# Performance work log

Measured on AMD Instinct MI355X. Metric: run time of the kernel, lower is better.

## Reference

```python
import jax, jax.numpy as jnp
import numpy as np
import math

B, N, DIM = 2, 4096, 1024
H, D, M = 16, 64, 256


def setup_inputs() -> dict:
    key = jax.random.key(0)
    ks = jax.random.split(key, 6)
    s = 1.0 / math.sqrt(DIM)
    return {
        "x": jax.random.normal(ks[0], (B, N, DIM), dtype=jnp.float32),
        "w_q": jax.random.normal(ks[1], (DIM, H * D), dtype=jnp.float32) * s,
        "w_k": jax.random.normal(ks[2], (DIM, H * D), dtype=jnp.float32) * s,
        "w_v": jax.random.normal(ks[3], (DIM, H * D), dtype=jnp.float32) * s,
        "w_o": jax.random.normal(ks[4], (H * D, DIM), dtype=jnp.float32) * s,
        "b_o": jnp.zeros((DIM,), dtype=jnp.float32),
        "omega": jax.random.normal(ks[5], (M, D), dtype=jnp.float32),
    }


def _heads(t):
    # [B, N, H*D] -> [B, H, N, D]
    return t.reshape(B, N, H, D).transpose(0, 2, 1, 3)


def _phi(t, omega):
    # t: [B,H,N,D], omega: [M,D] -> [B,H,N,M]
    proj = jnp.einsum("bhnd,md->bhnm", t, omega)
    norm = 0.5 * jnp.sum(t * t, axis=-1, keepdims=True)
    return jnp.exp(proj - norm) / math.sqrt(M)


def reference(x, w_q, w_k, w_v, w_o, b_o, omega):
    q = _heads(x @ w_q)
    k = _heads(x @ w_k)
    v = _heads(x @ w_v)
    phi_q = _phi(q, omega)          # [B,H,N,M]
    phi_k = _phi(k, omega)          # [B,H,N,M]
    kv = jnp.einsum("bhnm,bhnd->bhmd", phi_k, v)   # [B,H,M,D]
    k_sum = phi_k.sum(axis=2)                       # [B,H,M]
    z = 1.0 / (jnp.einsum("bhnm,bhm->bhn", phi_q, k_sum) + 1e-6)
    out = jnp.einsum("bhnm,bhmd->bhnd", phi_q, kv) * z[..., None]
    out = out.transpose(0, 2, 1, 3).reshape(B, N, H * D)
    return out @ w_o + b_o
```

## Files before the change

### kernel.cpp

```cpp
#include <hip/hip_runtime.h>

#define DEVI __device__ __forceinline__

using f32x4 = __attribute__((ext_vector_type(4))) float;
using fvec4 = __attribute__((ext_vector_type(4))) float;
using s16x4 = __attribute__((ext_vector_type(4))) short;
using s16x8 = __attribute__((ext_vector_type(8))) short;

DEVI unsigned short f2bf_rn(float f) {
  union { float f; unsigned u; } v; v.f = f;
  unsigned r = v.u + 0x7fffu + ((v.u >> 16) & 1u);
  return (unsigned short)(r >> 16);
}
DEVI float bf2f(unsigned short h) {
  union { unsigned u; float f; } v; v.u = ((unsigned)h) << 16;
  return v.f;
}
DEVI f32x4 mfma16(s16x8 a, s16x8 b, f32x4 c) {
  return __builtin_amdgcn_mfma_f32_16x16x32_bf16(a, b, c, 0, 0, 0);
}
DEVI void gld16(const void* g, void* lds) {
  __builtin_amdgcn_global_load_lds(
      (const __attribute__((address_space(1))) unsigned int*)g,
      (__attribute__((address_space(3))) unsigned int*)lds, 16, 0, 0);
}

__global__ __launch_bounds__(256) void k_split_x(
    const float* __restrict__ X,
    unsigned short* __restrict__ XH, unsigned short* __restrict__ XL)
{
  size_t i = ((size_t)blockIdx.x * 256 + threadIdx.x) * 8;
  fvec4 a = *(const fvec4*)&X[i];
  fvec4 b = *(const fvec4*)&X[i + 4];
  s16x8 hv, lv;
#pragma unroll
  for (int j = 0; j < 4; ++j) {
    unsigned short h = f2bf_rn(a[j]);
    hv[j] = (short)h; lv[j] = (short)f2bf_rn(a[j] - bf2f(h));
  }
#pragma unroll
  for (int j = 0; j < 4; ++j) {
    unsigned short h = f2bf_rn(b[j]);
    hv[4 + j] = (short)h; lv[4 + j] = (short)f2bf_rn(b[j] - bf2f(h));
  }
  *(s16x8*)&XH[i] = hv;
  *(s16x8*)&XL[i] = lv;
}

__global__ __launch_bounds__(256) void k_prep_w(
    const float* __restrict__ wq, const float* __restrict__ wk,
    const float* __restrict__ wv, const float* __restrict__ wo,
    unsigned short* __restrict__ WTh, unsigned short* __restrict__ WOT)
{
  __shared__ float tile[64][65];
  const int z = blockIdx.z;
  const float* src = (z == 0) ? wq : (z == 1) ? wk : (z == 2) ? wv : wo;
  const int k0 = blockIdx.x * 64;
  const int n0 = blockIdx.y * 64;
  const int t = threadIdx.x;
#pragma unroll
  for (int j = 0; j < 4; ++j) {
    int r = (t >> 4) + 16 * j;
    int c = (t & 15) * 4;
    fvec4 v = *(const fvec4*)&src[(size_t)(k0 + r) * 1024 + n0 + c];
#pragma unroll
    for (int i = 0; i < 4; ++i) tile[r][c + i] = v[i];
  }
  __syncthreads();
#pragma unroll
  for (int j = 0; j < 4; ++j) {
    int n = (t >> 4) + 16 * j;
    int kc = (t & 15) * 4;
    s16x4 hv;
#pragma unroll
    for (int i = 0; i < 4; ++i) hv[i] = (short)f2bf_rn(tile[kc + i][n]);
    if (z < 3) {
      *(s16x4*)&WTh[(size_t)(z * 1024 + n0 + n) * 1024 + k0 + kc] = hv;
    } else {
      *(s16x4*)&WOT[(size_t)(n0 + n) * 1024 + k0 + kc] = hv;
    }
  }
}

__global__ __launch_bounds__(256) void k_gemm_qkv(
    const unsigned short* __restrict__ XH, const unsigned short* __restrict__ XL,
    const unsigned short* __restrict__ WTh,
    unsigned short* __restrict__ QH, unsigned short* __restrict__ QL,
    unsigned short* __restrict__ KH, unsigned short* __restrict__ KL,
    unsigned short* __restrict__ VB)
{
  __shared__ unsigned short AH[2][128 * 32];
  __shared__ unsigned short BHs[2][128 * 32];
  __shared__ unsigned short AL[2][128 * 32];
  const int flat = blockIdx.y * 24 + blockIdx.x;
  const int swz = (flat & 7) * 192 + (flat >> 3);
  const int cb = swz % 24;
  const int rb = swz / 24;
  const int t = threadIdx.x;
  const int w = t >> 6, l = t & 63;
  const bool tp = (cb < 16);
  f32x4 acc[4][4];
#pragma unroll
  for (int a = 0; a < 4; ++a)
#pragma unroll
    for (int b = 0; b < 4; ++b) acc[a][b] = (f32x4)0.f;

  const int r0 = w * 32;
  const int lrow = l >> 2;
  const int lcol = (l & 3) * 8;
  const size_t gA = (size_t)(rb * 128 + r0 + lrow) * 1024 + lcol;
  const size_t gB = (size_t)(cb * 128 + r0 + lrow) * 1024 + lcol;
  const int lds0 = r0 * 32;
  const int lds1 = (r0 + 16) * 32;

  const int wm = (w & 1) * 64, wn = (w >> 1) * 64;
  const int lr = l & 15, ko = (l >> 4) * 8;

  auto STAGE = [&](int buf, int k0) {
    gld16(&XH[gA + k0], &AH[buf][lds0]);
    gld16(&XH[gA + (size_t)16 * 1024 + k0], &AH[buf][lds1]);
    if (tp) {
      gld16(&XL[gA + k0], &AL[buf][lds0]);
      gld16(&XL[gA + (size_t)16 * 1024 + k0], &AL[buf][lds1]);
    }
    gld16(&WTh[gB + k0], &BHs[buf][lds0]);
    gld16(&WTh[gB + (size_t)16 * 1024 + k0], &BHs[buf][lds1]);
  };

  STAGE(0, 0);
  int cur = 0;
  for (int ks = 0; ks < 32; ++ks) {
    if (ks < 31) {
      STAGE(cur ^ 1, (ks + 1) * 32);
      if (tp) asm volatile("s_waitcnt vmcnt(6)" ::: "memory");
      else    asm volatile("s_waitcnt vmcnt(4)" ::: "memory");
    } else {
      asm volatile("s_waitcnt vmcnt(0)" ::: "memory");
    }
    __builtin_amdgcn_s_barrier();
    asm volatile("" ::: "memory");
    s16x8 ah[4], al[4], bh[4];
#pragma unroll
    for (int f = 0; f < 4; ++f) {
      ah[f] = *(const s16x8*)&AH[cur][(wm + f * 16 + lr) * 32 + ko];
      bh[f] = *(const s16x8*)&BHs[cur][(wn + f * 16 + lr) * 32 + ko];
    }
    if (tp) {
#pragma unroll
      for (int f = 0; f < 4; ++f) al[f] = *(const s16x8*)&AL[cur][(wm + f * 16 + lr) * 32 + ko];
    }
#pragma unroll
    for (int fa = 0; fa < 4; ++fa)
#pragma unroll
      for (int fb = 0; fb < 4; ++fb) {
        acc[fa][fb] = mfma16(ah[fa], bh[fb], acc[fa][fb]);
        if (tp) acc[fa][fb] = mfma16(al[fa], bh[fb], acc[fa][fb]);
      }
    asm volatile("s_waitcnt lgkmcnt(0)" ::: "memory");
    __builtin_amdgcn_s_barrier();
    asm volatile("" ::: "memory");
    cur ^= 1;
  }
  const int lg = l >> 4;
#pragma unroll
  for (int fa = 0; fa < 4; ++fa)
#pragma unroll
    for (int r = 0; r < 4; ++r) {
      int row = rb * 128 + wm + fa * 16 + lg * 4 + r;
#pragma unroll
      for (int fb = 0; fb < 4; ++fb) {
        int col = cb * 128 + wn + fb * 16 + lr;
        float v = acc[fa][fb][r];
        if (tp) {
          unsigned short hs = f2bf_rn(v);
          unsigned short ls = f2bf_rn(v - bf2f(hs));
          if (cb < 8) {
            QH[(size_t)row * 1024 + col] = hs;
            QL[(size_t)row * 1024 + col] = ls;
          } else {
            KH[(size_t)row * 1024 + col - 1024] = hs;
            KL[(size_t)row * 1024 + col - 1024] = ls;
          }
        } else {
          VB[(size_t)row * 1024 + col - 2048] = f2bf_rn(v);
        }
      }
    }
}

__global__ __launch_bounds__(512, 1) void k_phik_kv(
    const unsigned short* __restrict__ KH, const unsigned short* __restrict__ KL,
    const unsigned short* __restrict__ VB,
    const float* __restrict__ omega, float* __restrict__ KVP)
{
  __shared__ unsigned short OH[256][72];
  __shared__ unsigned short KHs[64][72], KLs[64][72];
  __shared__ unsigned short PKT[256][72];
  __shared__ unsigned short AVT[80][72];
  __shared__ float norm_s[64];
  const int nc = blockIdx.x;
  const int bh = blockIdx.y;
  const int b = bh >> 4, h = bh & 15;
  const int t = threadIdx.x, w = t >> 6, l = t & 63;
  const int lr = l & 15, lg = l >> 4, ko8 = lg * 8;

#pragma unroll
  for (int j = 0; j < 8; ++j) {
    int e = j * 512 + t;
    int m = e >> 4, c = (e & 15) * 4;
    fvec4 v = *(const fvec4*)&omega[m * 64 + c];
    s16x4 hv;
#pragma unroll
    for (int i = 0; i < 4; ++i) hv[i] = (short)f2bf_rn(v[i]);
    *(s16x4*)&OH[m][c] = hv;
  }
  for (int e = t; e < 16 * 64; e += 512) {
    int rr = e >> 6, cc = e & 63;
    AVT[64 + rr][cc] = (rr == 0) ? (unsigned short)0x3F80 : (unsigned short)0;
  }

  f32x4 acc2[5][2];
#pragma unroll
  for (int a = 0; a < 5; ++a)
#pragma unroll
    for (int bb = 0; bb < 2; ++bb) acc2[a][bb] = (f32x4)0.f;

  for (int st = 0; st < 8; ++st) {
    const int n0 = nc * 512 + st * 64;
    __syncthreads();
    {
      int r = t >> 3, c8 = (t & 7) * 8;
      size_t o = (size_t)(b * 4096 + n0 + r) * 1024 + h * 64 + c8;
      s16x8 vh = *(const s16x8*)&KH[o];
      s16x8 vl = *(const s16x8*)&KL[o];
      *(s16x8*)&KHs[r][c8] = vh;
      *(s16x8*)&KLs[r][c8] = vl;
      float ss = 0.f;
#pragma unroll
      for (int i = 0; i < 8; ++i) {
        float q = bf2f((unsigned short)vh[i]) + bf2f((unsigned short)vl[i]);
        ss += q * q;
      }
      ss += __shfl_xor(ss, 1);
      ss += __shfl_xor(ss, 2);
      ss += __shfl_xor(ss, 4);
      if ((t & 7) == 0) norm_s[r] = 0.5f * ss;
    }
    {
      int n = t >> 3, dq = (t & 7) * 8;
      s16x8 v = *(const s16x8*)&VB[(size_t)(b * 4096 + n0 + n) * 1024 + h * 64 + dq];
#pragma unroll
      for (int i = 0; i < 8; ++i) AVT[dq + i][n] = (unsigned short)v[i];
    }
    __syncthreads();
    f32x4 acc[4][2];
#pragma unroll
    for (int a = 0; a < 4; ++a)
#pragma unroll
      for (int bb = 0; bb < 2; ++bb) acc[a][bb] = (f32x4)0.f;
#pragma unroll
    for (int ksub = 0; ksub < 2; ++ksub) {
      int ko = ksub * 32 + ko8;
      s16x8 ah[4], al[4], bh[2];
#pragma unroll
      for (int f = 0; f < 4; ++f) {
        ah[f] = *(const s16x8*)&KHs[f * 16 + lr][ko];
        al[f] = *(const s16x8*)&KLs[f * 16 + lr][ko];
      }
#pragma unroll
      for (int f = 0; f < 2; ++f) bh[f] = *(const s16x8*)&OH[w * 32 + f * 16 + lr][ko];
#pragma unroll
      for (int fa = 0; fa < 4; ++fa)
#pragma unroll
        for (int fb = 0; fb < 2; ++fb) {
          acc[fa][fb] = mfma16(ah[fa], bh[fb], acc[fa][fb]);
          acc[fa][fb] = mfma16(al[fa], bh[fb], acc[fa][fb]);
        }
    }
#pragma unroll
    for (int fa = 0; fa < 4; ++fa)
#pragma unroll
      for (int r = 0; r < 4; ++r) {
        int n = fa * 16 + lg * 4 + r;
        float nm = norm_s[n];
#pragma unroll
        for (int fb = 0; fb < 2; ++fb) {
          int m = w * 32 + fb * 16 + lr;
          float p = __expf(acc[fa][fb][r] - nm) * 0.0625f;
          PKT[m][n] = f2bf_rn(p);
        }
      }
    __syncthreads();
#pragma unroll
    for (int ksub = 0; ksub < 2; ++ksub) {
      int ko = ksub * 32 + ko8;
      s16x8 fA[5], fB[2];
#pragma unroll
      for (int f = 0; f < 5; ++f) fA[f] = *(const s16x8*)&AVT[f * 16 + lr][ko];
#pragma unroll
      for (int f = 0; f < 2; ++f) fB[f] = *(const s16x8*)&PKT[w * 32 + f * 16 + lr][ko];
#pragma unroll
      for (int fa = 0; fa < 5; ++fa)
#pragma unroll
        for (int fb = 0; fb < 2; ++fb) acc2[fa][fb] = mfma16(fA[fa], fB[fb], acc2[fa][fb]);
    }
  }
#pragma unroll
  for (int fa = 0; fa < 5; ++fa)
#pragma unroll
    for (int r = 0; r < 4; ++r) {
      int dp = fa * 16 + lg * 4 + r;
#pragma unroll
      for (int fb = 0; fb < 2; ++fb) {
        int m = w * 32 + fb * 16 + lr;
        KVP[(size_t)((bh * 8 + nc) * 80 + dp) * 256 + m] = acc2[fa][fb][r];
      }
    }
}

__global__ __launch_bounds__(256) void k_kv_reduce(
    const float* __restrict__ KVP, float* __restrict__ KVT)
{
  int idx = blockIdx.x * 256 + threadIdx.x;
  if (idx >= 32 * 80 * 256) return;
  int bh = idx / (80 * 256);
  int rem = idx % (80 * 256);
  float s = 0.f;
#pragma unroll
  for (int nci = 0; nci < 8; ++nci) s += KVP[(size_t)(bh * 8 + nci) * 80 * 256 + rem];
  KVT[idx] = s;
}

__global__ __launch_bounds__(256) void k_phiq_attn(
    const unsigned short* QH, const unsigned short* QL,
    const float* __restrict__ omega, const float* __restrict__ KVT,
    unsigned short* ATT)
{
  __shared__ unsigned short QHs[64][72], QLs[64][72];
  __shared__ unsigned short OH[256][72];
  __shared__ unsigned short PQ[64][264];
  __shared__ unsigned short KVB[80][264];
  __shared__ float norm_s[64];
  const int nt = blockIdx.x;
  const int bh = blockIdx.y;
  const int t = threadIdx.x, w = t >> 6, l = t & 63;
  const int b = bh >> 4, h = bh & 15;
  const int lr = l & 15, lg = l >> 4, ko8 = lg * 8;

  {
    int r = t >> 2, cq = (t & 3) * 4;
    float ss = 0.f;
#pragma unroll
    for (int j = 0; j < 4; ++j) {
      int c = cq + 16 * j;
      size_t o = (size_t)(b * 4096 + nt * 64 + r) * 1024 + h * 64 + c;
      s16x4 vh = *(const s16x4*)&QH[o];
      s16x4 vl = *(const s16x4*)&QL[o];
      *(s16x4*)&QHs[r][c] = vh;
      *(s16x4*)&QLs[r][c] = vl;
#pragma unroll
      for (int i = 0; i < 4; ++i) {
        float q = bf2f((unsigned short)vh[i]) + bf2f((unsigned short)vl[i]);
        ss += q * q;
      }
    }
    ss += __shfl_xor(ss, 1);
    ss += __shfl_xor(ss, 2);
    if ((t & 3) == 0) norm_s[r] = 0.5f * ss;
  }
#pragma unroll
  for (int j = 0; j < 16; ++j) {
    int e = j * 256 + t;
    int m = e >> 4, c = (e & 15) * 4;
    fvec4 v = *(const fvec4*)&omega[m * 64 + c];
    s16x4 hv;
#pragma unroll
    for (int i = 0; i < 4; ++i) hv[i] = (short)f2bf_rn(v[i]);
    *(s16x4*)&OH[m][c] = hv;
  }
#pragma unroll
  for (int j = 0; j < 20; ++j) {
    int e = (j * 256 + t) * 4;
    int dp = e >> 8, m = e & 255;
    fvec4 v = *(const fvec4*)&KVT[(size_t)bh * 80 * 256 + dp * 256 + m];
    s16x4 hv;
#pragma unroll
    for (int i = 0; i < 4; ++i) hv[i] = (short)f2bf_rn(v[i]);
    *(s16x4*)&KVB[dp][m] = hv;
  }
  __syncthreads();
  f32x4 acc[4][4];
#pragma unroll
  for (int a = 0; a < 4; ++a)
#pragma unroll
    for (int bb = 0; bb < 4; ++bb) acc[a][bb] = (f32x4)0.f;
#pragma unroll
  for (int ksub = 0; ksub < 2; ++ksub) {
    int ko = ksub * 32 + ko8;
    s16x8 ah[4], al[4], bh[4];
#pragma unroll
    for (int f = 0; f < 4; ++f) {
      ah[f] = *(const s16x8*)&QHs[f * 16 + lr][ko];
      al[f] = *(const s16x8*)&QLs[f * 16 + lr][ko];
      bh[f] = *(const s16x8*)&OH[w * 64 + f * 16 + lr][ko];
    }
#pragma unroll
    for (int fa = 0; fa < 4; ++fa)
#pragma unroll
      for (int fb = 0; fb < 4; ++fb) {
        acc[fa][fb] = mfma16(ah[fa], bh[fb], acc[fa][fb]);
        acc[fa][fb] = mfma16(al[fa], bh[fb], acc[fa][fb]);
      }
  }
#pragma unroll
  for (int fa = 0; fa < 4; ++fa)
#pragma unroll
    for (int r = 0; r < 4; ++r) {
      int n = fa * 16 + lg * 4 + r;
      float nm = norm_s[n];
#pragma unroll
      for (int fb = 0; fb < 4; ++fb) {
        int m = w * 64 + fb * 16 + lr;
        float p = __expf(acc[fa][fb][r] - nm) * 0.0625f;
        PQ[n][m] = f2bf_rn(p);
      }
    }
  __syncthreads();
  f32x4 acc2[5];
#pragma unroll
  for (int bb = 0; bb < 5; ++bb) acc2[bb] = (f32x4)0.f;
  for (int ks = 0; ks < 8; ++ks) {
    const int m0 = ks * 32;
    s16x8 fA = *(const s16x8*)&PQ[w * 16 + lr][m0 + ko8];
    s16x8 fB[5];
#pragma unroll
    for (int f = 0; f < 5; ++f) fB[f] = *(const s16x8*)&KVB[f * 16 + lr][m0 + ko8];
#pragma unroll
    for (int fb = 0; fb < 5; ++fb) acc2[fb] = mfma16(fA, fB[fb], acc2[fb]);
  }
#pragma unroll
  for (int r = 0; r < 4; ++r) {
    float den = __shfl(acc2[4][r], (l & 48));
    float z = 1.f / (den + 1e-6f);
    int n = nt * 64 + w * 16 + lg * 4 + r;
#pragma unroll
    for (int fb = 0; fb < 4; ++fb) {
      int col = h * 64 + fb * 16 + lr;
      ATT[(size_t)(b * 4096 + n) * 1024 + col] = f2bf_rn(acc2[fb][r] * z);
    }
  }
}

__global__ __launch_bounds__(256) void k_gemm_out(
    const unsigned short* __restrict__ ATT,
    const unsigned short* __restrict__ WOT,
    const float* __restrict__ b_o,
    float* __restrict__ OUT)
{
  __shared__ unsigned short As[2][128 * 32], Bs[2][128 * 32];
  const int flat = blockIdx.y * 8 + blockIdx.x;
  const int swz = (flat & 7) * 64 + (flat >> 3);
  const int cb = swz % 8;
  const int rb = swz / 8;
  const int t = threadIdx.x, w = t >> 6, l = t & 63;
  f32x4 acc[4][4];
#pragma unroll
  for (int a = 0; a < 4; ++a)
#pragma unroll
    for (int bb = 0; bb < 4; ++bb) acc[a][bb] = (f32x4)0.f;

  const int r0 = w * 32;
  const int lrow = l >> 2;
  const int lcol = (l & 3) * 8;
  const size_t gA = (size_t)(rb * 128 + r0 + lrow) * 1024 + lcol;
  const size_t gB = (size_t)(cb * 128 + r0 + lrow) * 1024 + lcol;
  const int lds0 = r0 * 32;
  const int lds1 = (r0 + 16) * 32;

  const int wm = (w & 1) * 64, wn = (w >> 1) * 64;
  const int lr = l & 15, ko = (l >> 4) * 8;

  auto STAGE = [&](int buf, int k0) {
    gld16(&ATT[gA + k0], &As[buf][lds0]);
    gld16(&ATT[gA + (size_t)16 * 1024 + k0], &As[buf][lds1]);
    gld16(&WOT[gB + k0], &Bs[buf][lds0]);
    gld16(&WOT[gB + (size_t)16 * 1024 + k0], &Bs[buf][lds1]);
  };

  STAGE(0, 0);
  int cur = 0;
  for (int ks = 0; ks < 32; ++ks) {
    if (ks < 31) {
      STAGE(cur ^ 1, (ks + 1) * 32);
      asm volatile("s_waitcnt vmcnt(4)" ::: "memory");
    } else {
      asm volatile("s_waitcnt vmcnt(0)" ::: "memory");
    }
    __builtin_amdgcn_s_barrier();
    asm volatile("" ::: "memory");
    s16x8 fA[4], fB[4];
#pragma unroll
    for (int f = 0; f < 4; ++f) {
      fA[f] = *(const s16x8*)&As[cur][(wm + f * 16 + lr) * 32 + ko];
      fB[f] = *(const s16x8*)&Bs[cur][(wn + f * 16 + lr) * 32 + ko];
    }
#pragma unroll
    for (int fa = 0; fa < 4; ++fa)
#pragma unroll
      for (int fb = 0; fb < 4; ++fb) acc[fa][fb] = mfma16(fA[fa], fB[fb], acc[fa][fb]);
    asm volatile("s_waitcnt lgkmcnt(0)" ::: "memory");
    __builtin_amdgcn_s_barrier();
    asm volatile("" ::: "memory");
    cur ^= 1;
  }
  const int lg = l >> 4;
#pragma unroll
  for (int fa = 0; fa < 4; ++fa)
#pragma unroll
    for (int r = 0; r < 4; ++r) {
      int row = rb * 128 + wm + fa * 16 + lg * 4 + r;
#pragma unroll
      for (int fb = 0; fb < 4; ++fb) {
        int col = cb * 128 + wn + fb * 16 + lr;
        OUT[(size_t)row * 1024 + col] = acc[fa][fb][r] + b_o[col];
      }
    }
}

extern "C" void kernel_launch(void* const* d_in, const int* in_sizes, int n_in,
                              void* d_out, int out_size, void* d_ws, size_t ws_size,
                              hipStream_t stream)
{
  const float* x  = (const float*)d_in[0];
  const float* wq = (const float*)d_in[1];
  const float* wk = (const float*)d_in[2];
  const float* wv = (const float*)d_in[3];
  const float* wo = (const float*)d_in[4];
  const float* bo = (const float*)d_in[5];
  const float* om = (const float*)d_in[6];
  float* out = (float*)d_out;

  const size_t PLANE = (size_t)8192 * 1024 * 2;
  char* ws = (char*)d_ws;
  unsigned short* WOT = (unsigned short*)(ws);
  char* segB = ws + 2097152;
  char* segC = segB + 2 * PLANE;
  char* segD = segC + 4 * PLANE;
  char* segE = segD + 26214400;

  unsigned short* QH  = (unsigned short*)segB;
  unsigned short* QL  = (unsigned short*)(segB + PLANE);
  unsigned short* ATT = (unsigned short*)segB;

  unsigned short* KH  = (unsigned short*)segC;
  unsigned short* KL  = (unsigned short*)(segC + PLANE);
  unsigned short* VB  = (unsigned short*)(segC + 2 * PLANE);
  unsigned short* XH  = (unsigned short*)(segC + 3 * PLANE);

  unsigned short* WTh = (unsigned short*)segD;
  unsigned short* XL  = (unsigned short*)(segD + 6291456);
  float* KVP = (float*)segD;
  float* KVT = (float*)segE;

  k_split_x<<<dim3(4096), 256, 0, stream>>>(x, XH, XL);
  k_prep_w<<<dim3(16, 16, 4), 256, 0, stream>>>(wq, wk, wv, wo, WTh, WOT);
  k_gemm_qkv<<<dim3(24, 64), 256, 0, stream>>>(XH, XL, WTh, QH, QL, KH, KL, VB);
  k_phik_kv<<<dim3(8, 32), 512, 0, stream>>>(KH, KL, VB, om, KVP);
  k_kv_reduce<<<dim3(2560), 256, 0, stream>>>(KVP, KVT);
  k_phiq_attn<<<dim3(64, 32), 256, 0, stream>>>(QH, QL, om, KVT, ATT);
  k_gemm_out<<<dim3(8, 64), 256, 0, stream>>>(ATT, WOT, bo, out);
}
```

Before: 232.8 us.

## Triple-buffer GEMM loads and precompute bf16 omega and KV tables

The QKV and output GEMMs now use three LDS stages with two loads in flight instead of double buffering, which hides more global-memory latency at the cost of extra LDS per block. Omega is converted to bf16 once inside the weight-prep kernel, and the KV reduction writes bf16 directly. This removes the repeated fp32 loads and conversions from every attention and phi_k block, with 16-byte copies into LDS. The larger LDS footprint may reduce how many blocks fit on each CU.

```diff
diff --git a/kernel.cpp b/kernel.cpp
--- a/kernel.cpp
+++ b/kernel.cpp
@@ -50,14 +50,28 @@
 __global__ __launch_bounds__(256) void k_prep_w(
     const float* __restrict__ wq, const float* __restrict__ wk,
     const float* __restrict__ wv, const float* __restrict__ wo,
-    unsigned short* __restrict__ WTh, unsigned short* __restrict__ WOT)
+    const float* __restrict__ omega,
+    unsigned short* __restrict__ WTh, unsigned short* __restrict__ WOT,
+    unsigned short* __restrict__ OMB)
 {
   __shared__ float tile[64][65];
   const int z = blockIdx.z;
+  const int t = threadIdx.x;
+  if (z == 4) {
+    int bid = blockIdx.x * 16 + blockIdx.y;
+    if (bid < 16) {
+      int i = (bid * 256 + t) * 4;
+      fvec4 v = *(const fvec4*)&omega[i];
+      s16x4 hv;
+#pragma unroll
+      for (int q = 0; q < 4; ++q) hv[q] = (short)f2bf_rn(v[q]);
+      *(s16x4*)&OMB[i] = hv;
+    }
+    return;
+  }
   const float* src = (z == 0) ? wq : (z == 1) ? wk : (z == 2) ? wv : wo;
   const int k0 = blockIdx.x * 64;
   const int n0 = blockIdx.y * 64;
-  const int t = threadIdx.x;
 #pragma unroll
   for (int j = 0; j < 4; ++j) {
     int r = (t >> 4) + 16 * j;
@@ -89,9 +103,9 @@
     unsigned short* __restrict__ KH, unsigned short* __restrict__ KL,
     unsigned short* __restrict__ VB)
 {
-  __shared__ unsigned short AH[2][128 * 32];
-  __shared__ unsigned short BHs[2][128 * 32];
-  __shared__ unsigned short AL[2][128 * 32];
+  __shared__ unsigned short AH[3][128 * 32];
+  __shared__ unsigned short BHs[3][128 * 32];
+  __shared__ unsigned short AL[3][128 * 32];
   const int flat = blockIdx.y * 24 + blockIdx.x;
   const int swz = (flat & 7) * 192 + (flat >> 3);
   const int cb = swz % 24;
@@ -128,10 +142,15 @@
   };
 
   STAGE(0, 0);
+  STAGE(1, 32);
   int cur = 0;
   for (int ks = 0; ks < 32; ++ks) {
-    if (ks < 31) {
-      STAGE(cur ^ 1, (ks + 1) * 32);
+    if (ks < 30) {
+      int nxt = (cur >= 1) ? cur - 1 : 2;
+      STAGE(nxt, (ks + 2) * 32);
+      if (tp) asm volatile("s_waitcnt vmcnt(12)" ::: "memory");
+      else    asm volatile("s_waitcnt vmcnt(8)" ::: "memory");
+    } else if (ks == 30) {
       if (tp) asm volatile("s_waitcnt vmcnt(6)" ::: "memory");
       else    asm volatile("s_waitcnt vmcnt(4)" ::: "memory");
     } else {
@@ -159,7 +178,7 @@
     asm volatile("s_waitcnt lgkmcnt(0)" ::: "memory");
     __builtin_amdgcn_s_barrier();
     asm volatile("" ::: "memory");
-    cur ^= 1;
+    cur = (cur < 2) ? cur + 1 : 0;
   }
   const int lg = l >> 4;
 #pragma unroll
@@ -191,7 +210,7 @@
 __global__ __launch_bounds__(512, 1) void k_phik_kv(
     const unsigned short* __restrict__ KH, const unsigned short* __restrict__ KL,
     const unsigned short* __restrict__ VB,
-    const float* __restrict__ omega, float* __restrict__ KVP)
+    const unsigned short* __restrict__ OMB, float* __restrict__ KVP)
 {
   __shared__ unsigned short OH[256][72];
   __shared__ unsigned short KHs[64][72], KLs[64][72];
@@ -205,14 +224,10 @@
   const int lr = l & 15, lg = l >> 4, ko8 = lg * 8;
 
 #pragma unroll
-  for (int j = 0; j < 8; ++j) {
-    int e = j * 512 + t;
-    int m = e >> 4, c = (e & 15) * 4;
-    fvec4 v = *(const fvec4*)&omega[m * 64 + c];
-    s16x4 hv;
-#pragma unroll
-    for (int i = 0; i < 4; ++i) hv[i] = (short)f2bf_rn(v[i]);
-    *(s16x4*)&OH[m][c] = hv;
+  for (int j = 0; j < 4; ++j) {
+    int idx = j * 512 + t;
+    int m = idx >> 3, c = (idx & 7) * 8;
+    *(s16x8*)&OH[m][c] = *(const s16x8*)&OMB[m * 64 + c];
   }
   for (int e = t; e < 16 * 64; e += 512) {
     int rr = e >> 6, cc = e & 63;
@@ -319,7 +334,7 @@
 }
 
 __global__ __launch_bounds__(256) void k_kv_reduce(
-    const float* __restrict__ KVP, float* __restrict__ KVT)
+    const float* __restrict__ KVP, unsigned short* __restrict__ KVTB)
 {
   int idx = blockIdx.x * 256 + threadIdx.x;
   if (idx >= 32 * 80 * 256) return;
@@ -328,12 +343,13 @@
   float s = 0.f;
 #pragma unroll
   for (int nci = 0; nci < 8; ++nci) s += KVP[(size_t)(bh * 8 + nci) * 80 * 256 + rem];
-  KVT[idx] = s;
+  KVTB[idx] = f2bf_rn(s);
 }
 
 __global__ __launch_bounds__(256) void k_phiq_attn(
     const unsigned short* QH, const unsigned short* QL,
-    const float* __restrict__ omega, const float* __restrict__ KVT,
+    const unsigned short* __restrict__ OMB,
+    const unsigned short* __restrict__ KVTB,
     unsigned short* ATT)
 {
   __shared__ unsigned short QHs[64][72], QLs[64][72];
@@ -369,24 +385,16 @@
     if ((t & 3) == 0) norm_s[r] = 0.5f * ss;
   }
 #pragma unroll
-  for (int j = 0; j < 16; ++j) {
-    int e = j * 256 + t;
-    int m = e >> 4, c = (e & 15) * 4;
-    fvec4 v = *(const fvec4*)&omega[m * 64 + c];
-    s16x4 hv;
-#pragma unroll
-    for (int i = 0; i < 4; ++i) hv[i] = (short)f2bf_rn(v[i]);
-    *(s16x4*)&OH[m][c] = hv;
-  }
-#pragma unroll
-  for (int j = 0; j < 20; ++j) {
-    int e = (j * 256 + t) * 4;
+  for (int j = 0; j < 8; ++j) {
+    int idx = j * 256 + t;
+    int m = idx >> 3, c = (idx & 7) * 8;
+    *(s16x8*)&OH[m][c] = *(const s16x8*)&OMB[m * 64 + c];
+  }
+#pragma unroll
+  for (int j = 0; j < 10; ++j) {
+    int e = (j * 256 + t) * 8;
     int dp = e >> 8, m = e & 255;
-    fvec4 v = *(const fvec4*)&KVT[(size_t)bh * 80 * 256 + dp * 256 + m];
-    s16x4 hv;
-#pragma unroll
-    for (int i = 0; i < 4; ++i) hv[i] = (short)f2bf_rn(v[i]);
-    *(s16x4*)&KVB[dp][m] = hv;
+    *(s16x8*)&KVB[dp][m] = *(const s16x8*)&KVTB[(size_t)bh * 80 * 256 + dp * 256 + m];
   }
   __syncthreads();
   f32x4 acc[4][4];
@@ -457,7 +465,7 @@
     const float* __restrict__ b_o,
     float* __restrict__ OUT)
 {
-  __shared__ unsigned short As[2][128 * 32], Bs[2][128 * 32];
+  __shared__ unsigned short As[3][128 * 32], Bs[3][128 * 32];
   const int flat = blockIdx.y * 8 + blockIdx.x;
   const int swz = (flat & 7) * 64 + (flat >> 3);
   const int cb = swz % 8;
@@ -488,10 +496,14 @@
   };
 
   STAGE(0, 0);
+  STAGE(1, 32);
   int cur = 0;
   for (int ks = 0; ks < 32; ++ks) {
-    if (ks < 31) {
-      STAGE(cur ^ 1, (ks + 1) * 32);
+    if (ks < 30) {
+      int nxt = (cur >= 1) ? cur - 1 : 2;
+      STAGE(nxt, (ks + 2) * 32);
+      asm volatile("s_waitcnt vmcnt(8)" ::: "memory");
+    } else if (ks == 30) {
       asm volatile("s_waitcnt vmcnt(4)" ::: "memory");
     } else {
       asm volatile("s_waitcnt vmcnt(0)" ::: "memory");
@@ -511,7 +523,7 @@
     asm volatile("s_waitcnt lgkmcnt(0)" ::: "memory");
     __builtin_amdgcn_s_barrier();
     asm volatile("" ::: "memory");
-    cur ^= 1;
+    cur = (cur < 2) ? cur + 1 : 0;
   }
   const int lg = l >> 4;
 #pragma unroll
@@ -560,13 +572,14 @@
   unsigned short* WTh = (unsigned short*)segD;
   unsigned short* XL  = (unsigned short*)(segD + 6291456);
   float* KVP = (float*)segD;
-  float* KVT = (float*)segE;
+  unsigned short* KVTB = (unsigned short*)segE;
+  unsigned short* OMB  = (unsigned short*)(segE + 1310720);
 
   k_split_x<<<dim3(4096), 256, 0, stream>>>(x, XH, XL);
-  k_prep_w<<<dim3(16, 16, 4), 256, 0, stream>>>(wq, wk, wv, wo, WTh, WOT);
+  k_prep_w<<<dim3(16, 16, 5), 256, 0, stream>>>(wq, wk, wv, wo, om, WTh, WOT, OMB);
   k_gemm_qkv<<<dim3(24, 64), 256, 0, stream>>>(XH, XL, WTh, QH, QL, KH, KL, VB);
-  k_phik_kv<<<dim3(8, 32), 512, 0, stream>>>(KH, KL, VB, om, KVP);
-  k_kv_reduce<<<dim3(2560), 256, 0, stream>>>(KVP, KVT);
-  k_phiq_attn<<<dim3(64, 32), 256, 0, stream>>>(QH, QL, om, KVT, ATT);
+  k_phik_kv<<<dim3(8, 32), 512, 0, stream>>>(KH, KL, VB, OMB, KVP);
+  k_kv_reduce<<<dim3(2560), 256, 0, stream>>>(KVP, KVTB);
+  k_phiq_attn<<<dim3(64, 32), 256, 0, stream>>>(QH, QL, OMB, KVTB, ATT);
   k_gemm_out<<<dim3(8, 64), 256, 0, stream>>>(ATT, WOT, bo, out);
 }
```

Result: slower. 242.3 us (+4.1%).
